# Kernel tuning notes

Hardware: AMD Instinct MI355X
Metric: run time of the kernel (lower is better)

## Reference

```python
import jax, jax.numpy as jnp
import numpy as np

DIM = 512
HEADS = 8
DH = 64
LANDMARKS = 256
PINV_ITERS = 6
K = 4
BUF = 256


def _ln(x, g, b, eps=1e-5):
    mu = x.mean(-1, keepdims=True)
    var = ((x - mu) ** 2).mean(-1, keepdims=True)
    return (x - mu) / jnp.sqrt(var + eps) * g + b


def _pinv(a):
    # Moore-Penrose iterative pseudo-inverse (lucidrains nystrom_attention)
    aa = jnp.abs(a)
    z = jnp.swapaxes(a, -1, -2) / (aa.sum(-1).max() * aa.sum(-2).max())
    I = jnp.eye(a.shape[-1], dtype=a.dtype)
    for _ in range(PINV_ITERS):
        az = a @ z
        z = 0.25 * z @ (13.0 * I - az @ (15.0 * I - az @ (7.0 * I - az)))
    return z


def _nystrom(x, qkv_w, out_w, out_b, res_k):
    b, n, _ = x.shape
    rem = n % LANDMARKS
    if rem > 0:
        x = jnp.pad(x, ((0, 0), (LANDMARKS - rem, 0), (0, 0)))  # left-pad seq
    npad = x.shape[1]
    qkv = x @ qkv_w.T
    q, k, v = jnp.split(qkv, 3, axis=-1)
    split_heads = lambda t: t.reshape(b, npad, HEADS, DH).transpose(0, 2, 1, 3)
    q = split_heads(q) * (DH ** -0.5)
    k = split_heads(k)
    v = split_heads(v)
    l = npad // LANDMARKS
    q_l = q.reshape(b, HEADS, LANDMARKS, l, DH).mean(3)
    k_l = k.reshape(b, HEADS, LANDMARKS, l, DH).mean(3)
    a1 = jax.nn.softmax(jnp.einsum('bhnd,bhmd->bhnm', q, k_l), axis=-1)
    a2 = jax.nn.softmax(jnp.einsum('bhmd,bhkd->bhmk', q_l, k_l), axis=-1)
    a3 = jax.nn.softmax(jnp.einsum('bhmd,bhnd->bhmn', q_l, k), axis=-1)
    out = (a1 @ _pinv(a2)) @ (a3 @ v)  # (b,h,npad,dh)
    # depthwise residual conv over seq dim, one channel per head
    out = out + jax.lax.conv_general_dilated(
        v, res_k, (1, 1), ((16, 16), (0, 0)),
        dimension_numbers=('NCHW', 'OIHW', 'NCHW'), feature_group_count=HEADS)
    out = out.transpose(0, 2, 1, 3).reshape(b, npad, DIM) @ out_w.T + out_b
    return out[:, -n:]


def _dwconv(x, w, b, pad):
    y = jax.lax.conv_general_dilated(
        x, w, (1, 1), ((pad, pad), (pad, pad)),
        dimension_numbers=('NCHW', 'OIHW', 'NCHW'), feature_group_count=DIM)
    return y + b[None, :, None, None]


def _leaky(t):
    return jnp.where(t >= 0, t, 0.01 * t)


def reference(x, fc1_w, fc1_b, cls_token, ln1_g, ln1_b, qkv1_w, out1_w, out1_b, res1_k,
              ppeg_w7, ppeg_b7, ppeg_w5, ppeg_b5, ppeg_w3, ppeg_b3,
              ln2_g, ln2_b, qkv2_w, out2_w, out2_b, res2_k, norm_g, norm_b, fc2_w, fc2_b,
              dsl_w1, dsl_b1, dsl_w2, dsl_b2,
              gcn_w1, gcn_we, gcn_b1, gcn_w2, gcn_b2,
              gcn_head_w, gcn_head_b, gcn_dist_w, gcn_dist_b, rehearsal):
    B, N, _ = x.shape
    h = jax.nn.relu(x @ fc1_w.T + fc1_b)                 # (B,N,512)
    Hs = int(np.ceil(np.sqrt(N)))                        # square-grid side
    add = Hs * Hs - N
    h = jnp.concatenate([h, h[:, :add]], axis=1)         # wrap-pad to Hs*Hs
    h = jnp.concatenate([jnp.broadcast_to(cls_token, (B, 1, DIM)), h], axis=1)
    h = h + _nystrom(_ln(h, ln1_g, ln1_b), qkv1_w, out1_w, out1_b, res1_k)
    cls, feat = h[:, :1], h[:, 1:]
    cnn = feat.transpose(0, 2, 1).reshape(B, DIM, Hs, Hs)
    cnn = cnn + _dwconv(cnn, ppeg_w7, ppeg_b7, 3) + _dwconv(cnn, ppeg_w5, ppeg_b5, 2) + _dwconv(cnn, ppeg_w3, ppeg_b3, 1)
    h = jnp.concatenate([cls, cnn.reshape(B, DIM, -1).transpose(0, 2, 1)], axis=1)
    h = h + _nystrom(_ln(h, ln2_g, ln2_b), qkv2_w, out2_w, out2_b, res2_k)
    h = _ln(h, norm_g, norm_b)[:, 0]                     # (B,512) cls embedding
    logits_mlp = h @ fc2_w.T + fc2_b
    # rehearsal concat -> buffer of BUF nodes
    x_concat = jnp.concatenate([h, rehearsal], axis=0)[:BUF]
    # DSL: MLP + cosine KNN graph + scatter_mean edge_attr
    xg = _leaky(_leaky(x_concat @ dsl_w1.T + dsl_b1) @ dsl_w2.T + dsl_b2)
    xn = xg / jnp.linalg.norm(xg, axis=-1, keepdims=True)
    _, idx = jax.lax.top_k(xn @ xn.T, K)                 # (BUF,K) cosine KNN incl self
    edge_attr = xg[idx].mean(1)                          # scatter_mean over incoming edges
    # 2-layer GCN over the KNN graph (mean aggregation + edge_attr injection)
    h1 = jax.nn.relu((xg + edge_attr) @ gcn_w1.T + edge_attr @ gcn_we.T + gcn_b1)
    h2 = (h1 + h1[idx].mean(1)) @ gcn_w2.T + gcn_b2
    logits_graph = h2[:B] @ gcn_head_w.T + gcn_head_b
    logits_distill = h1[:B] @ gcn_dist_w.T + gcn_dist_b
    return logits_mlp, logits_graph, logits_distill


def setup_inputs() -> dict:
    key = jax.random.key(0)
    ks = jax.random.split(key, 24)
    r = lambda i, shp, s=0.02: jax.random.normal(ks[i], shp, dtype=jnp.float32) * s
    z = lambda shp: jnp.zeros(shp, dtype=jnp.float32)
    o = lambda shp: jnp.ones(shp, dtype=jnp.float32)
    return {
        'x': jax.random.normal(ks[0], (2, 4096, 512), dtype=jnp.float32),
        'fc1_w': r(1, (512, 512)), 'fc1_b': z((512,)),
        'cls_token': r(2, (1, 1, 512), 1.0),
        'ln1_g': o((512,)), 'ln1_b': z((512,)),
        'qkv1_w': r(3, (1536, 512)), 'out1_w': r(4, (512, 512)), 'out1_b': z((512,)),
        'res1_k': r(5, (8, 1, 33, 1)),
        'ppeg_w7': r(6, (512, 1, 7, 7)), 'ppeg_b7': z((512,)),
        'ppeg_w5': r(7, (512, 1, 5, 5)), 'ppeg_b5': z((512,)),
        'ppeg_w3': r(8, (512, 1, 3, 3)), 'ppeg_b3': z((512,)),
        'ln2_g': o((512,)), 'ln2_b': z((512,)),
        'qkv2_w': r(9, (1536, 512)), 'out2_w': r(10, (512, 512)), 'out2_b': z((512,)),
        'res2_k': r(11, (8, 1, 33, 1)),
        'norm_g': o((512,)), 'norm_b': z((512,)),
        'fc2_w': r(12, (2, 512)), 'fc2_b': z((2,)),
        'dsl_w1': r(13, (256, 512)), 'dsl_b1': z((256,)),
        'dsl_w2': r(14, (512, 256)), 'dsl_b2': z((512,)),
        'gcn_w1': r(15, (512, 512)), 'gcn_we': r(16, (512, 512)), 'gcn_b1': z((512,)),
        'gcn_w2': r(17, (512, 512)), 'gcn_b2': z((512,)),
        'gcn_head_w': r(18, (2, 512)), 'gcn_head_b': z((2,)),
        'gcn_dist_w': r(19, (2, 512)), 'gcn_dist_b': z((2,)),
        'rehearsal': jax.random.uniform(ks[20], (256, 512), dtype=jnp.float32),
    }
```

## Files before the change

kernel.cpp:

```cpp
#include <hip/hip_runtime.h>
#include <math.h>

#define BB 2
#define NSEQ 4096
#define N1 4097
#define NPAD 4352
#define PADR 255
#define DIM 512
#define NH 8
#define DH 64
#define LM 256
#define NT 1536

typedef short bf16x8 __attribute__((ext_vector_type(8)));
typedef float f32x4 __attribute__((ext_vector_type(4)));

__device__ __forceinline__ unsigned short f2bf(float x){
  unsigned int u = __float_as_uint(x);
  unsigned int r = (u + 0x7FFFu + ((u >> 16) & 1u)) >> 16;
  return (unsigned short)r;
}
__device__ __forceinline__ float bf2f(unsigned short h){
  return __uint_as_float(((unsigned int)h) << 16);
}
// ... 138 lines not shown

#define DOMFMA2(AH_, AL_, BH_, BL_) do {                               \
    _Pragma("unroll")                                                  \
    for (int i = 0; i < 2; ++i)                                        \
      _Pragma("unroll")                                                \
      for (int j = 0; j < 2; ++j) {                                    \
        acc[i][j] = __builtin_amdgcn_mfma_f32_16x16x32_bf16(AH_[i], BH_[j], acc[i][j], 0,0,0); \
        acc[i][j] = __builtin_amdgcn_mfma_f32_16x16x32_bf16(AH_[i], BL_[j], acc[i][j], 0,0,0); \
        acc[i][j] = __builtin_amdgcn_mfma_f32_16x16x32_bf16(AL_[i], BH_[j], acc[i][j], 0,0,0); \
      } } while (0)

  LDF2(A0h, A0l, B0h, B0l, 0);
  for (int ks = 0; ks < 256; ks += 64) {
    LDF2(A1h, A1l, B1h, B1l, ks + 32);
    DOMFMA2(A0h, A0l, B0h, B0l);
    if (ks + 64 < 256) LDF2(A0h, A0l, B0h, B0l, ks + 64);
    DOMFMA2(A1h, A1l, B1h, B1l);
  }
#undef LDF2
#undef DOMFMA2

  int crb = (l >> 4) << 2;
  #pragma unroll
  for (int i = 0; i < 2; ++i) {
    int rbase = row0 + i*16 + crb;
    #pragma unroll
    for (int j = 0; j < 2; ++j) {
      int colg = col0 + j*16 + lr;
      float v[4];
      #pragma unroll
      for (int r = 0; r < 4; ++r)
        v[r] = alpha * acc[i][j][r] + (((rbase + r) == colg) ? diag : 0.f);
      if (C32) {
        #pragma unroll
        for (int r = 0; r < 4; ++r) C32[offC + (size_t)(rbase + r) * N + colg] = v[r];
      }
      if (CH) {
        #pragma unroll
        for (int r = 0; r < 4; ++r) {
          unsigned short hh = f2bf(v[r]);
          CH[offC + (size_t)(rbase + r) * N + colg] = hh;
          CL[offC + (size_t)(rbase + r) * N + colg] = f2bf(v[r] - bf2f(hh));
        }
      }
      if (CTH) {
        ushort4 th, tl;
        unsigned short* ph = (unsigned short*)&th;
        unsigned short* pl = (unsigned short*)&tl;
        #pragma unroll
        for (int r = 0; r < 4; ++r) { ph[r] = f2bf(v[r]); pl[r] = f2bf(v[r] - bf2f(ph[r])); }
        *(ushort4*)&CTH[offT + (size_t)colg * 256 + rbase] = th;
        *(ushort4*)&CTL[offT + (size_t)colg * 256 + rbase] = tl;
      }
      if (DTH) {
        ushort4 th, tl;
        unsigned short* ph = (unsigned short*)&th;
        unsigned short* pl = (unsigned short*)&tl;
        #pragma unroll
        for (int r = 0; r < 4; ++r) {
          float dv = (((rbase + r) == colg) ? diag2 : 0.f) - v[r];
          ph[r] = f2bf(dv); pl[r] = f2bf(dv - bf2f(ph[r]));
        }
        *(ushort4*)&DTH[offT + (size_t)colg * 256 + rbase] = th;
        *(ushort4*)&DTL[offT + (size_t)colg * 256 + rbase] = tl;
      }
    }
  }
}

__global__ void split_k(const float* __restrict__ src, unsigned short* __restrict__ dh,
                        unsigned short* __restrict__ dl, int n4){
  int i = blockIdx.x * 256 + threadIdx.x;
  if (i >= n4) return;
  float4 v = ((const float4*)src)[i];
  ushort4 H, L;
  H.x = f2bf(v.x); L.x = f2bf(v.x - bf2f(H.x));
  H.y = f2bf(v.y); L.y = f2bf(v.y - bf2f(H.y));
  H.z = f2bf(v.z); L.z = f2bf(v.z - bf2f(H.z));
  H.w = f2bf(v.w); L.w = f2bf(v.w - bf2f(H.w));
  ((ushort4*)dh)[i] = H;
  ((ushort4*)dl)[i] = L;
}

__global__ void z0_split(const float* __restrict__ a2, const float* __restrict__ scal,
                         unsigned short* __restrict__ zH, unsigned short* __restrict__ zL,
                         unsigned short* __restrict__ zTH, unsigned short* __restrict__ zTL){
  size_t idx = (size_t)blockIdx.x * 256 + threadIdx.x;
  size_t bh = idx >> 16;
  int rc = (int)(idx & 65535);
  int r = rc >> 8, c = rc & 255;
  float v = a2[idx] * scal[32];
  unsigned short hh = f2bf(v), ll = f2bf(v - bf2f(hh));
  zTH[idx] = hh; zTL[idx] = ll;
  size_t tidx = (bh << 16) + (size_t)c * 256 + r;
  zH[tidx] = hh; zL[tidx] = ll;
}

__global__ void split_T_av(const float* __restrict__ av,
                           unsigned short* __restrict__ TH, unsigned short* __restrict__ TL){
  size_t idx = (size_t)blockIdx.x * 256 + threadIdx.x;
  size_t bh = idx >> 14;
  int md = (int)(idx & 16383);
  int m = md >> 6, d = md & 63;
  float v = av[idx];
  unsigned short hh = f2bf(v);
  size_t tix = (bh << 14) + (size_t)d * 256 + m;
  TH[tix] = hh; TL[tix] = f2bf(v - bf2f(hh));
}

__global__ __launch_bounds__(256) void ln_pad_split(const float* __restrict__ hsrc,
    unsigned short* __restrict__ dH, unsigned short* __restrict__ dL,
    const float* __restrict__ g, const float* __restrict__ bt){
  __shared__ double red[256];
  int row = blockIdx.x;
  int b = row / NPAD, r = row % NPAD;
  unsigned short* rh = dH + (size_t)row * DIM;
  unsigned short* rl = dL + (size_t)row * DIM;
  int t = threadIdx.x;
  if (r < PADR) { rh[t] = 0; rh[t+256] = 0; rl[t] = 0; rl[t+256] = 0; return; }
  const float* x = hsrc + ((size_t)b * N1 + (r - PADR)) * DIM;
  double x0 = (double)x[t], x1 = (double)x[t + 256];
  double mu = blk_sumd(x0 + x1, red) * (1.0/512.0);
  double d0 = x0 - mu, d1 = x1 - mu;
  double var = blk_sumd(d0*d0 + d1*d1, red) * (1.0/512.0);
  double inv = 1.0 / sqrt(var + 1e-5);
  float y0 = (float)(d0 * inv * (double)g[t]       + (double)bt[t]);
  float y1 = (float)(d1 * inv * (double)g[t + 256] + (double)bt[t + 256]);
  unsigned short h0 = f2bf(y0), h1 = f2bf(y1);
  rh[t] = h0;       rl[t] = f2bf(y0 - bf2f(h0));
  rh[t + 256] = h1; rl[t + 256] = f2bf(y1 - bf2f(h1));
}

__global__ void landmark(const float* __restrict__ qkv, float* __restrict__ ql, float* __restrict__ kl){
  int blk = blockIdx.x;
  int bh = blk >> 8, m = blk & 255;
  int b = bh >> 3, hh = bh & 7;
  int d = threadIdx.x;
  float sq = 0.f, sk = 0.f;
  for (int l = 0; l < 17; ++l) {
    size_t o = ((size_t)b * NPAD + m * 17 + l) * NT + hh * 64 + d;
    sq += qkv[o];
    sk += qkv[o + 512];
  }
  ql[((size_t)bh * 256 + m) * 64 + d] = 0.125f * sq / 17.f;
  kl[((size_t)bh * 256 + m) * 64 + d] = sk / 17.f;
}

__global__ __launch_bounds__(256) void transpose_kl(const float* __restrict__ kl, float* __restrict__ klT){
  __shared__ float tile[64][65];
  int bh = blockIdx.y;
  int m0 = blockIdx.x * 64;
  int t = threadIdx.x;
  for (int i = t; i < 4096; i += 256) {
    int r = i >> 6, c = i & 63;
    tile[r][c] = kl[((size_t)bh * 256 + m0 + r) * 64 + c];
  }
  __syncthreads();
  float* kb = klT + (size_t)bh * 64 * 256;
  for (int i = t; i < 4096; i += 256) {
    int d = i >> 6, mm = i & 63;
    kb[(size_t)d * 256 + m0 + mm] = tile[mm][d];
  }
}

__global__ __launch_bounds__(256) void a2_kernel(const float* __restrict__ ql, const float* __restrict__ klT,
                                                 float* __restrict__ a2){
  __shared__ float qs[64]; __shared__ float red[256];
  int blk = blockIdx.x;
  int bh = blk >> 8, i = blk & 255;
  int t = threadIdx.x;
  if (t < 64) qs[t] = ql[((size_t)bh * 256 + i) * 64 + t];
  __syncthreads();
  const float* kb = klT + (size_t)bh * 16384;
  float s = 0.f;
  #pragma unroll
  for (int d = 0; d < 64; ++d) s += qs[d] * kb[d * 256 + t];
  float mx = blk_max(s, red);
  float e = expf(s - mx);
  float sum = blk_sum(e, red);
  a2[((size_t)bh * 256 + i) * 256 + t] = e / sum;
}

__global__ __launch_bounds__(256) void colrow_max(const float* __restrict__ a2, float* __restrict__ scal){
  __shared__ float red[256];
  int bh = blockIdx.x, t = threadIdx.x;
  const float* A = a2 + (size_t)bh * 65536;
  float cs = 0.f, rs = 0.f;
  for (int i = 0; i < 256; ++i) cs += A[(size_t)i * 256 + t];
  for (int j = 0; j < 256; ++j) rs += A[(size_t)t * 256 + j];
  float cmax = blk_max(cs, red);
  float rmax = blk_max(rs, red);
  if (t == 0) { scal[bh] = cmax; scal[16 + bh] = rmax; }
}
__global__ void scal_red(float* scal){
  if (threadIdx.x == 0) {
    float cm = scal[0], rm = scal[16];
    for (int i = 1; i < 16; ++i) { cm = fmaxf(cm, scal[i]); rm = fmaxf(rm, scal[16 + i]); }
    scal[32] = 1.f / (rm * cm);
  }
}

__global__ __launch_bounds__(256) void fa3v_kernel(const float* __restrict__ qkv, const float* __restrict__ ql,
                                                   float* __restrict__ accp, float* __restrict__ mlp){
  int part = blockIdx.x, qt = blockIdx.y, bh = blockIdx.z;
  int b = bh >> 3, hh = bh & 7;
  int t = threadIdx.x;
  int w = t >> 6, l = t & 63;
  int lr = l & 15, lk = (l >> 4) << 3;
  int w16 = w * 16;
  int crb = (l >> 4) << 2;
  __shared__ unsigned short KH[64][72], KL[64][72];
  __shared__ unsigned short PH[64][72], PL[64][72];
  __shared__ float Ss[64][68];
  __shared__ float redm[64][4];
  __shared__ float mrow[64], lrow[64], scales[64];
  bf16x8 qh[2], qlo[2];
  {
    const float* qrow = ql + ((size_t)bh * 256 + qt * 64 + w16 + lr) * 64;
    #pragma unroll
    for (int s = 0; s < 2; ++s) {
      #pragma unroll
      for (int e = 0; e < 8; ++e) {
        float v = qrow[s * 32 + lk + e];
        unsigned short hv = f2bf(v);
        qh[s][e]  = (short)hv;
        qlo[s][e] = (short)f2bf(v - bf2f(hv));
      }
    }
  }
  if (t < 64) { mrow[t] = -3.4e38f; lrow[t] = 0.f; }
  f32x4 acc[4];
  #pragma unroll
  for (int j = 0; j < 4; ++j) acc[j] = (f32x4){0.f,0.f,0.f,0.f};
  __syncthreads();
  int rr = t >> 2, sg = (t & 3) << 4;
  for (int tile = 0; tile < 4; ++tile) {
    int nbase = part * 256 + tile * 64;
    for (int i = t; i < 4096; i += 256) {
      int r = i >> 6, c = i & 63;
      float v = qkv[((size_t)b * NPAD + nbase + r) * NT + 512 + hh * 64 + c];
      unsigned short hv = f2bf(v);
      KH[r][c] = hv; KL[r][c] = f2bf(v - bf2f(hv));
    }
    __syncthreads();
    #pragma unroll
    for (int j = 0; j < 4; ++j) {
      f32x4 sf = (f32x4){0.f,0.f,0.f,0.f};
      #pragma unroll
      for (int s = 0; s < 2; ++s) {
        bf16x8 kh8 = *(const bf16x8*)&KH[j*16 + lr][s*32 + lk];
        bf16x8 kl8 = *(const bf16x8*)&KL[j*16 + lr][s*32 + lk];
        sf = __builtin_amdgcn_mfma_f32_16x16x32_bf16(qh[s],  kh8, sf, 0,0,0);
        sf = __builtin_amdgcn_mfma_f32_16x16x32_bf16(qh[s],  kl8, sf, 0,0,0);
        sf = __builtin_amdgcn_mfma_f32_16x16x32_bf16(qlo[s], kh8, sf, 0,0,0);
      }
      #pragma unroll
      for (int r = 0; r < 4; ++r) Ss[w16 + crb + r][j*16 + lr] = sf[r];
    }
    __syncthreads();
    for (int i = t; i < 4096; i += 256) {
      int r = i >> 6, c = i & 63;
      float v = qkv[((size_t)b * NPAD + nbase + r) * NT + 1024 + hh * 64 + c];
      unsigned short hv = f2bf(v);
      KH[c][r] = hv; KL[c][r] = f2bf(v - bf2f(hv));
    }
    float lm = -3.4e38f;
    #pragma unroll
    for (int c = 0; c < 16; ++c) lm = fmaxf(lm, Ss[rr][sg + c]);
    redm[rr][t & 3] = lm;
    float mold = mrow[rr];
    float rm = fmaxf(fmaxf(redm[rr][0], redm[rr][1]), fmaxf(redm[rr][2], redm[rr][3]));
    float mnew = fmaxf(mold, rm);
    float sc_r = expf(mold - mnew);
    if ((t & 3) == 0) { scales[rr] = sc_r; mrow[rr] = mnew; }
    float ls = 0.f;
    #pragma unroll
    for (int c = 0; c < 16; ++c) {
      float p = expf(Ss[rr][sg + c] - mnew);
      unsigned short hv = f2bf(p);
      PH[rr][sg + c] = hv; PL[rr][sg + c] = f2bf(p - bf2f(hv));
      ls += p;
    }
    redm[rr][t & 3] = ls;
    __syncthreads();
    if ((t & 3) == 0) lrow[rr] = lrow[rr] * sc_r + redm[rr][0]+redm[rr][1]+redm[rr][2]+redm[rr][3];
    {
      float s0 = scales[w16 + crb], s1 = scales[w16 + crb + 1],
            s2 = scales[w16 + crb + 2], s3 = scales[w16 + crb + 3];
      #pragma unroll
      for (int j = 0; j < 4; ++j) { acc[j][0]*=s0; acc[j][1]*=s1; acc[j][2]*=s2; acc[j][3]*=s3; }
    }
    bf16x8 pah[2], pal[2];
    #pragma unroll
    for (int s = 0; s < 2; ++s) {
      pah[s] = *(const bf16x8*)&PH[w16 + lr][s*32 + lk];
      pal[s] = *(const bf16x8*)&PL[w16 + lr][s*32 + lk];
    }
    #pragma unroll
    for (int j = 0; j < 4; ++j) {
      #pragma unroll
      for (int s = 0; s < 2; ++s) {
        bf16x8 vh = *(const bf16x8*)&KH[j*16 + lr][s*32 + lk];
        bf16x8 vl = *(const bf16x8*)&KL[j*16 + lr][s*32 + lk];
        acc[j] = __builtin_amdgcn_mfma_f32_16x16x32_bf16(pah[s], vh, acc[j], 0,0,0);
        acc[j] = __builtin_amdgcn_mfma_f32_16x16x32_bf16(pah[s], vl, acc[j], 0,0,0);
        acc[j] = __builtin_amdgcn_mfma_f32_16x16x32_bf16(pal[s], vh, acc[j], 0,0,0);
      }
    }
    __syncthreads();
  }
  int blk = (bh * 4 + qt) * 17 + part;
  float* ap = accp + (size_t)blk * 4096;
  #pragma unroll
  for (int j = 0; j < 4; ++j)
    #pragma unroll
    for (int r = 0; r < 4; ++r)
      ap[(w16 + crb + r) * 64 + j*16 + lr] = acc[j][r];
  if (t < 64) { mlp[(size_t)blk*128 + t] = mrow[t]; mlp[(size_t)blk*128 + 64 + t] = lrow[t]; }
}

__global__ __launch_bounds__(256) void fa3v_combine(const float* __restrict__ accp, const float* __restrict__ mlp,
                                                    float* __restrict__ av){
  int g = blockIdx.x;
  int t = threadIdx.x;
  int r = t >> 2, sg = (t & 3) << 4;
  int bh = g >> 2, qt = g & 3;
  float mp[17], lp[17];
  #pragma unroll
  for (int p = 0; p < 17; ++p) {
    mp[p] = mlp[(size_t)(g*17+p)*128 + r];
    lp[p] = mlp[(size_t)(g*17+p)*128 + 64 + r];
  }
  float M = mp[0];
  #pragma unroll
  for (int p = 1; p < 17; ++p) M = fmaxf(M, mp[p]);
  float w[17]; float L = 0.f;
  #pragma unroll
  for (int p = 0; p < 17; ++p) { w[p] = expf(mp[p] - M); L += w[p] * lp[p]; }
  float invL = 1.f / L;
  #pragma unroll
  for (int c = 0; c < 16; ++c) {
    float s = 0.f;
    #pragma unroll
    for (int p = 0; p < 17; ++p) s += w[p] * accp[(size_t)(g*17+p)*4096 + r*64 + sg + c];
    av[((size_t)(bh*256 + qt*64 + r))*64 + sg + c] = s * invL;
  }
}

__global__ __launch_bounds__(256) void fa1_kernel(const float* __restrict__ qkv, const float* __restrict__ kl,
                                                  const float* __restrict__ zav, float* __restrict__ merged,
                                                  unsigned short* __restrict__ merH,
                                                  unsigned short* __restrict__ merL){
  int nt = blockIdx.x, bh = blockIdx.y;
  int b = bh >> 3, hh = bh & 7;
  int t = threadIdx.x;
  int w = t >> 6, l = t & 63;
  int lr = l & 15, lk = (l >> 4) << 3;
  int w16 = w * 16;
  int crb = (l >> 4) << 2;
  int n0 = nt * 64;
  __shared__ unsigned short KH[64][72], KL[64][72];
  __shared__ unsigned short PH[64][72], PL[64][72];
  __shared__ float Ss[64][68];
  __shared__ float redm[64][4];
  __shared__ float mrow[64], lrow[64], scales[64];
  bf16x8 qh[2], qlo[2];
  {
    const float* qrow = qkv + ((size_t)b * NPAD + n0 + w16 + lr) * NT + hh * 64;
    #pragma unroll
    for (int s = 0; s < 2; ++s) {
      #pragma unroll
      for (int e = 0; e < 8; ++e) {
        float v = 0.125f * qrow[s * 32 + lk + e];
        unsigned short hv = f2bf(v);
        qh[s][e]  = (short)hv;
        qlo[s][e] = (short)f2bf(v - bf2f(hv));
      }
    }
  }
  if (t < 64) { mrow[t] = -3.4e38f; lrow[t] = 0.f; }
  f32x4 acc[4];
  #pragma unroll
  for (int j = 0; j < 4; ++j) acc[j] = (f32x4){0.f,0.f,0.f,0.f};
  __syncthreads();
  int rr = t >> 2, sg = (t & 3) << 4;
  for (int tile = 0; tile < 4; ++tile) {
    int mbase = tile * 64;
    for (int i = t; i < 4096; i += 256) {
      int r = i >> 6, c = i & 63;
      float v = kl[((size_t)bh * 256 + mbase + r) * 64 + c];
      unsigned short hv = f2bf(v);
      KH[r][c] = hv; KL[r][c] = f2bf(v - bf2f(hv));
    }
    __syncthreads();
    #pragma unroll
    for (int j = 0; j < 4; ++j) {
      f32x4 sf = (f32x4){0.f,0.f,0.f,0.f};
      #pragma unroll
      for (int s = 0; s < 2; ++s) {
        bf16x8 kh8 = *(const bf16x8*)&KH[j*16 + lr][s*32 + lk];
        bf16x8 kl8 = *(const bf16x8*)&KL[j*16 + lr][s*32 + lk];
        sf = __builtin_amdgcn_mfma_f32_16x16x32_bf16(qh[s],  kh8, sf, 0,0,0);
        sf = __builtin_amdgcn_mfma_f32_16x16x32_bf16(qh[s],  kl8, sf, 0,0,0);
        sf = __builtin_amdgcn_mfma_f32_16x16x32_bf16(qlo[s], kh8, sf, 0,0,0);
      }
      #pragma unroll
      for (int r = 0; r < 4; ++r) Ss[w16 + crb + r][j*16 + lr] = sf[r];
    }
    __syncthreads();
    for (int i = t; i < 4096; i += 256) {
      int r = i >> 6, c = i & 63;
      float v = zav[((size_t)bh * 256 + mbase + r) * 64 + c];
      unsigned short hv = f2bf(v);
      KH[c][r] = hv; KL[c][r] = f2bf(v - bf2f(hv));
    }
    float lm = -3.4e38f;
    #pragma unroll
    for (int c = 0; c < 16; ++c) lm = fmaxf(lm, Ss[rr][sg + c]);
    redm[rr][t & 3] = lm;
    float mold = mrow[rr];
    float rm = fmaxf(fmaxf(redm[rr][0], redm[rr][1]), fmaxf(redm[rr][2], redm[rr][3]));
    float mnew = fmaxf(mold, rm);
    float sc_r = expf(mold - mnew);
    if ((t & 3) == 0) { scales[rr] = sc_r; mrow[rr] = mnew; }
    float ls = 0.f;
    #pragma unroll
    for (int c = 0; c < 16; ++c) {
      float p = expf(Ss[rr][sg + c] - mnew);
      unsigned short hv = f2bf(p);
      PH[rr][sg + c] = hv; PL[rr][sg + c] = f2bf(p - bf2f(hv));
      ls += p;
    }
    redm[rr][t & 3] = ls;
    __syncthreads();
    if ((t & 3) == 0) lrow[rr] = lrow[rr] * sc_r + redm[rr][0]+redm[rr][1]+redm[rr][2]+redm[rr][3];
    {
      float s0 = scales[w16 + crb], s1 = scales[w16 + crb + 1],
            s2 = scales[w16 + crb + 2], s3 = scales[w16 + crb + 3];
      #pragma unroll
      for (int j = 0; j < 4; ++j) { acc[j][0]*=s0; acc[j][1]*=s1; acc[j][2]*=s2; acc[j][3]*=s3; }
    }
    bf16x8 pah[2], pal[2];
    #pragma unroll
    for (int s = 0; s < 2; ++s) {
      pah[s] = *(const bf16x8*)&PH[w16 + lr][s*32 + lk];
      pal[s] = *(const bf16x8*)&PL[w16 + lr][s*32 + lk];
    }
    #pragma unroll
    for (int j = 0; j < 4; ++j) {
      #pragma unroll
      for (int s = 0; s < 2; ++s) {
        bf16x8 vh = *(const bf16x8*)&KH[j*16 + lr][s*32 + lk];
        bf16x8 vl = *(const bf16x8*)&KL[j*16 + lr][s*32 + lk];
        acc[j] = __builtin_amdgcn_mfma_f32_16x16x32_bf16(pah[s], vh, acc[j], 0,0,0);
        acc[j] = __builtin_amdgcn_mfma_f32_16x16x32_bf16(pah[s], vl, acc[j], 0,0,0);
        acc[j] = __builtin_amdgcn_mfma_f32_16x16x32_bf16(pal[s], vh, acc[j], 0,0,0);
      }
    }
    __syncthreads();
  }
  #pragma unroll
  for (int r = 0; r < 4; ++r) {
    float invl = 1.f / lrow[w16 + crb + r];
    size_t rowoff = ((size_t)b * NPAD + n0 + w16 + crb + r) * DIM + hh * 64;
    float* mp = &merged[rowoff];
    #pragma unroll
    for (int j = 0; j < 4; ++j) {
      float v = mp[j*16 + lr] + acc[j][r] * invl;
      mp[j*16 + lr] = v;
      unsigned short hv = f2bf(v);
      merH[rowoff + j*16 + lr] = hv;
      merL[rowoff + j*16 + lr] = f2bf(v - bf2f(hv));
    }
  }
}

__global__ __launch_bounds__(256) void conv_res(const float* __restrict__ qkv, const float* __restrict__ rk,
                                                float* __restrict__ merged){
  __shared__ float vt[288][16];
  __shared__ float rks[33];
  int n0 = blockIdx.x * 256;
  int c0 = blockIdx.y * 16;
  int b  = blockIdx.z;
  int t = threadIdx.x;
  int hh = c0 >> 6;
  if (t < 33) rks[t] = rk[hh * 33 + t];
  for (int i = t; i < 288 * 4; i += 256) {
    int sp = i >> 2, q = (i & 3) << 2;
    int n = n0 - 16 + sp;
    float4 v = make_float4(0.f,0.f,0.f,0.f);
    if (n >= 0 && n < NPAD)
      v = *(const float4*)&qkv[((size_t)b * NPAD + n) * NT + 1024 + c0 + q];
    vt[sp][q] = v.x; vt[sp][q+1] = v.y; vt[sp][q+2] = v.z; vt[sp][q+3] = v.w;
  }
  __syncthreads();
  int c = t & 15, g = t >> 4;
  for (int m = 0; m < 16; ++m) {
// ... 92 lines not shown
  __shared__ double red[256];
  int i = blockIdx.x, t = threadIdx.x;
  double a = (double)xg[(size_t)i * 512 + t], b = (double)xg[(size_t)i * 512 + t + 256];
  double s = blk_sumd(a*a + b*b, red);
  if (t == 0) rn[i] = sqrt(s);
}

__global__ __launch_bounds__(256) void topk_k(const float* __restrict__ xg, const double* __restrict__ rn,
                                              int* __restrict__ idxb){
  __shared__ double sc[256]; __shared__ double redv[256]; __shared__ int redi[256];
  int i = blockIdx.x, j = threadIdx.x;
  const float* xi = xg + (size_t)i * 512;
  const float* xj = xg + (size_t)j * 512;
  double s = 0.;
  for (int c = 0; c < 512; ++c) s += (double)xi[c] * (double)xj[c];
  s /= (rn[i] * rn[j]);
  sc[j] = s; __syncthreads();
  for (int r = 0; r < 4; ++r) {
    redv[j] = sc[j]; redi[j] = j; __syncthreads();
    for (int st = 128; st > 0; st >>= 1) {
      if (j < st) {
        if (redv[j + st] > redv[j] || (redv[j + st] == redv[j] && redi[j + st] < redi[j])) {
          redv[j] = redv[j + st]; redi[j] = redi[j + st];
        }
      }
      __syncthreads();
    }
    if (j == 0) { idxb[i * 4 + r] = redi[0]; sc[redi[0]] = -1e300; }
    __syncthreads();
  }
}

__global__ void edge_k_split(const float* __restrict__ xg, const int* __restrict__ idxb,
                             float* __restrict__ edge,
                             unsigned short* __restrict__ eH, unsigned short* __restrict__ eL){
  size_t idx = (size_t)blockIdx.x * 256 + threadIdx.x;
  int i = (int)(idx >> 9), c = (int)(idx & 511);
  const int* id = idxb + i * 4;
  float v = 0.25f * (xg[(size_t)id[0]*512 + c] + xg[(size_t)id[1]*512 + c] +
                     xg[(size_t)id[2]*512 + c] + xg[(size_t)id[3]*512 + c]);
  edge[idx] = v;
  unsigned short hh = f2bf(v);
  eH[idx] = hh; eL[idx] = f2bf(v - bf2f(hh));
}
__global__ void vadd_split(const float* __restrict__ a, const float* __restrict__ b,
                           unsigned short* __restrict__ oH, unsigned short* __restrict__ oL){
  size_t idx = (size_t)blockIdx.x * 256 + threadIdx.x;
  float v = a[idx] + b[idx];
  unsigned short hh = f2bf(v);
  oH[idx] = hh; oL[idx] = f2bf(v - bf2f(hh));
}
__global__ void h1gather_split(const float* __restrict__ h1, const int* __restrict__ idxb,
                               unsigned short* __restrict__ oH, unsigned short* __restrict__ oL){
  size_t idx = (size_t)blockIdx.x * 256 + threadIdx.x;
  int i = (int)(idx >> 9), c = (int)(idx & 511);
  const int* id = idxb + i * 4;
  float v = h1[idx] + 0.25f * (h1[(size_t)id[0]*512 + c] + h1[(size_t)id[1]*512 + c] +
                               h1[(size_t)id[2]*512 + c] + h1[(size_t)id[3]*512 + c]);
  unsigned short hh = f2bf(v);
  oH[idx] = hh; oL[idx] = f2bf(v - bf2f(hh));
}

__global__ void logits2(const float* __restrict__ src, const float* __restrict__ w,
                        const float* __restrict__ bias, float* __restrict__ out){
  int rc = blockIdx.x; int r = rc >> 1, c = rc & 1;
  int t = threadIdx.x;
  double s = 0.;
  for (int k = t; k < 512; k += 64) s += (double)src[(size_t)r * 512 + k] * (double)w[(size_t)c * 512 + k];
  for (int off = 32; off > 0; off >>= 1) s += __shfl_down(s, off);
  if (t == 0) out[rc] = (float)(s + (double)bias[c]);
}

__global__ void sentinel_k(float* out){ if (threadIdx.x < 12) out[threadIdx.x] = 1e30f; }

struct NysBufs {
  float *qkv, *ql, *kl, *klT, *av, *zav, *merged;
  float *a2f32, *scal, *accp, *mlp;
  unsigned short *padH, *padL, *merH, *merL, *wqH, *wqL, *owH, *owL;
  unsigned short *a2H, *a2L;
  unsigned short *zAH, *zAL, *zATH, *zATL;
  unsigned short *zBH, *zBL, *zBTH, *zBTL;
  unsigned short *azH, *azL, *t1TH, *t1TL, *t2TH, *t2TL;
  unsigned short *avTH, *avTL;
};

static void run_nystrom(hipStream_t stream, float* hbuf,
                        const float* lng, const float* lnb, const float* qkvw,
                        const float* outw, const float* outb, const float* rk,
                        const NysBufs& w)
{
  ln_pad_split<<<BB * NPAD, 256, 0, stream>>>(hbuf, w.padH, w.padL, lng, lnb);
  split_k<<<(NT * DIM / 4 + 255) / 256, 256, 0, stream>>>(qkvw, w.wqH, w.wqL, NT * DIM / 4);
  gemm_mfma<<<dim3(NT/128, (BB*NPAD)/128), 256, 0, stream>>>(w.padH, w.padL, w.wqH, w.wqL,
                                                             nullptr, nullptr, w.qkv,
                                                             BB*NPAD, NT, DIM, 0, nullptr, nullptr);
  landmark<<<BB * NH * LM, 64, 0, stream>>>(w.qkv, w.ql, w.kl);
  transpose_kl<<<dim3(LM/64, 16), 256, 0, stream>>>(w.kl, w.klT);
  fa3v_kernel<<<dim3(17, 4, 16), 256, 0, stream>>>(w.qkv, w.ql, w.accp, w.mlp);
  fa3v_combine<<<64, 256, 0, stream>>>(w.accp, w.mlp, w.av);
  split_T_av<<<1024, 256, 0, stream>>>(w.av, w.avTH, w.avTL);
  a2_kernel<<<BB * NH * LM, 256, 0, stream>>>(w.ql, w.klT, w.a2f32);
  colrow_max<<<16, 256, 0, stream>>>(w.a2f32, w.scal);
  scal_red<<<1, 64, 0, stream>>>(w.scal);
  split_k<<<(16 * 65536 / 4 + 255) / 256, 256, 0, stream>>>(w.a2f32, w.a2H, w.a2L, 16 * 65536 / 4);
  z0_split<<<4096, 256, 0, stream>>>(w.a2f32, w.scal, w.zAH, w.zAL, w.zATH, w.zATL);
  const unsigned short *zcH = w.zAH, *zcL = w.zAL, *zcTH = w.zATH, *zcTL = w.zATL;
  unsigned short *znH = w.zBH, *znL = w.zBL, *znTH = w.zBTH, *znTL = w.zBTL;
  for (int it = 0; it < 6; ++it) {
    mm_mfma<<<dim3(8,8,16), 64, 0, stream>>>(w.a2H, w.a2L, zcTH, zcTL,
        w.azH, w.azL, nullptr, nullptr, w.t1TH, w.t1TL, nullptr, 256, 1.f, 0.f, 7.f);
    mm_mfma<<<dim3(8,8,16), 64, 0, stream>>>(w.azH, w.azL, w.t1TH, w.t1TL,
        nullptr, nullptr, w.t2TH, w.t2TL, nullptr, nullptr, nullptr, 256, -1.f, 15.f, 0.f);
    mm_mfma<<<dim3(8,8,16), 64, 0, stream>>>(w.azH, w.azL, w.t2TH, w.t2TL,
        nullptr, nullptr, w.t1TH, w.t1TL, nullptr, nullptr, nullptr, 256, -1.f, 13.f, 0.f);
    mm_mfma<<<dim3(8,8,16), 64, 0, stream>>>(zcH, zcL, w.t1TH, w.t1TL,
        znH, znL, znTH, znTL, nullptr, nullptr, nullptr, 256, 0.25f, 0.f, 0.f);
    const unsigned short* t;
    t = zcH; zcH = znH; znH = (unsigned short*)t;
    t = zcL; zcL = znL; znL = (unsigned short*)t;
    t = zcTH; zcTH = znTH; znTH = (unsigned short*)t;
    t = zcTL; zcTL = znTL; znTL = (unsigned short*)t;
  }
  mm_mfma<<<dim3(2,8,16), 64, 0, stream>>>(zcH, zcL, w.avTH, w.avTL,
      nullptr, nullptr, nullptr, nullptr, nullptr, nullptr, w.zav, 64, 1.f, 0.f, 0.f);
  conv_res<<<dim3(17, 32, 2), 256, 0, stream>>>(w.qkv, rk, w.merged);
  fa1_kernel<<<dim3(NPAD/64, 16), 256, 0, stream>>>(w.qkv, w.kl, w.zav, w.merged, w.merH, w.merL);
  split_k<<<(DIM*DIM/4 + 255) / 256, 256, 0, stream>>>(outw, w.owH, w.owL, DIM*DIM/4);
  for (int b = 0; b < BB; ++b)
    gemm_mfma<<<dim3(DIM/128, (N1+127)/128), 256, 0, stream>>>(
        w.merH + ((size_t)b*NPAD + PADR)*DIM, w.merL + ((size_t)b*NPAD + PADR)*DIM,
        w.owH, w.owL, outb,
        hbuf + (size_t)b*N1*DIM, hbuf + (size_t)b*N1*DIM,
        N1, DIM, DIM, 0, nullptr, nullptr);
}

extern "C" void kernel_launch(void* const* d_in, const int* in_sizes, int n_in,
                              void* d_out, int out_size, void* d_ws, size_t ws_size,
                              hipStream_t stream) {
  (void)in_sizes; (void)n_in; (void)out_size;
  const float* x        = (const float*)d_in[0];
  const float* fc1_w    = (const float*)d_in[1];
  const float* fc1_b    = (const float*)d_in[2];
  const float* cls_tok  = (const float*)d_in[3];
  const float* ln1_g    = (const float*)d_in[4];
  const float* ln1_b    = (const float*)d_in[5];
  const float* qkv1_w   = (const float*)d_in[6];
  const float* out1_w   = (const float*)d_in[7];
  const float* out1_b   = (const float*)d_in[8];
  const float* res1_k   = (const float*)d_in[9];
  const float* ppeg_w7  = (const float*)d_in[10];
  const float* ppeg_b7  = (const float*)d_in[11];
  const float* ppeg_w5  = (const float*)d_in[12];
  const float* ppeg_b5  = (const float*)d_in[13];
  const float* ppeg_w3  = (const float*)d_in[14];
  const float* ppeg_b3  = (const float*)d_in[15];
  const float* ln2_g    = (const float*)d_in[16];
  const float* ln2_b    = (const float*)d_in[17];
  const float* qkv2_w   = (const float*)d_in[18];
  const float* out2_w   = (const float*)d_in[19];
  const float* out2_b   = (const float*)d_in[20];
  const float* res2_k   = (const float*)d_in[21];
  const float* norm_g   = (const float*)d_in[22];
  const float* norm_b   = (const float*)d_in[23];
  const float* fc2_w    = (const float*)d_in[24];
  const float* fc2_b    = (const float*)d_in[25];
  const float* dsl_w1   = (const float*)d_in[26];
  const float* dsl_b1   = (const float*)d_in[27];
  const float* dsl_w2   = (const float*)d_in[28];
  const float* dsl_b2   = (const float*)d_in[29];
  const float* gcn_w1   = (const float*)d_in[30];
  const float* gcn_we   = (const float*)d_in[31];
  const float* gcn_b1   = (const float*)d_in[32];
  const float* gcn_w2   = (const float*)d_in[33];
  const float* gcn_b2   = (const float*)d_in[34];
  const float* gcn_hw   = (const float*)d_in[35];
  const float* gcn_hb   = (const float*)d_in[36];
  const float* gcn_dw   = (const float*)d_in[37];
  const float* gcn_db   = (const float*)d_in[38];
  const float* rehearsal= (const float*)d_in[39];
  float* out = (float*)d_out;

  char* base = (char*)d_ws;
  size_t off = 0;
  auto takeb = [&](size_t bytes) { void* p = base + off; off += (bytes + 255) & ~(size_t)255; return p; };

  float* h    = (float*)takeb((size_t)BB * N1 * DIM * 4);
  float* h2   = (float*)takeb((size_t)BB * N1 * DIM * 4);
  NysBufs nb;
  nb.padH   = (unsigned short*)takeb((size_t)BB * NPAD * DIM * 2);
  nb.padL   = (unsigned short*)takeb((size_t)BB * NPAD * DIM * 2);
  nb.qkv    = (float*)takeb((size_t)BB * NPAD * NT * 4);
  nb.ql     = (float*)takeb((size_t)BB * NH * LM * DH * 4);
  nb.kl     = (float*)takeb((size_t)BB * NH * LM * DH * 4);
  nb.klT    = (float*)takeb((size_t)BB * NH * LM * DH * 4);
  nb.av     = (float*)takeb((size_t)BB * NH * LM * DH * 4);
  nb.zav    = (float*)takeb((size_t)BB * NH * LM * DH * 4);
  nb.merged = (float*)takeb((size_t)BB * NPAD * DIM * 4);
  nb.merH   = (unsigned short*)takeb((size_t)BB * NPAD * DIM * 2);
  nb.merL   = (unsigned short*)takeb((size_t)BB * NPAD * DIM * 2);
  nb.wqH    = (unsigned short*)takeb((size_t)NT * DIM * 2);
  nb.wqL    = (unsigned short*)takeb((size_t)NT * DIM * 2);
  nb.owH    = (unsigned short*)takeb((size_t)DIM * DIM * 2);
  nb.owL    = (unsigned short*)takeb((size_t)DIM * DIM * 2);
  nb.avTH   = (unsigned short*)takeb((size_t)16 * 64 * 256 * 2);
  nb.avTL   = (unsigned short*)takeb((size_t)16 * 64 * 256 * 2);
  nb.scal   = (float*)takeb(64 * 4);
  nb.mlp    = (float*)takeb((size_t)1088 * 128 * 4);
  float* hcls = (float*)takeb((size_t)BB * DIM * 4);
  float* xg1  = (float*)takeb((size_t)256 * 256 * 4);
  float* xg   = (float*)takeb((size_t)256 * 512 * 4);
  double* rn  = (double*)takeb(256 * 8);
  int*   idxb = (int*)takeb(1024 * 4);
  float* edge = (float*)takeb((size_t)256 * 512 * 4);
  float* h1g  = (float*)takeb((size_t)256 * 512 * 4);
  float* h2g  = (float*)takeb((size_t)256 * 512 * 4);
  unsigned short* xcH   = (unsigned short*)takeb((size_t)256 * 512 * 2);
  unsigned short* xcL   = (unsigned short*)takeb((size_t)256 * 512 * 2);
  unsigned short* dw1H  = (unsigned short*)takeb((size_t)256 * 512 * 2);
  unsigned short* dw1L  = (unsigned short*)takeb((size_t)256 * 512 * 2);
  unsigned short* xg1H  = (unsigned short*)takeb((size_t)256 * 256 * 2);
  unsigned short* xg1L  = (unsigned short*)takeb((size_t)256 * 256 * 2);
  unsigned short* dw2H  = (unsigned short*)takeb((size_t)512 * 256 * 2);
  unsigned short* dw2L  = (unsigned short*)takeb((size_t)512 * 256 * 2);
  unsigned short* h1pH  = (unsigned short*)takeb((size_t)256 * 512 * 2);
  unsigned short* h1pL  = (unsigned short*)takeb((size_t)256 * 512 * 2);
  unsigned short* gw1H  = (unsigned short*)takeb((size_t)512 * 512 * 2);
  unsigned short* gw1L  = (unsigned short*)takeb((size_t)512 * 512 * 2);
  unsigned short* edgeH = (unsigned short*)takeb((size_t)256 * 512 * 2);
  unsigned short* edgeL = (unsigned short*)takeb((size_t)256 * 512 * 2);
  unsigned short* gweH  = (unsigned short*)takeb((size_t)512 * 512 * 2);
  unsigned short* gweL  = (unsigned short*)takeb((size_t)512 * 512 * 2);
  unsigned short* h1p2H = (unsigned short*)takeb((size_t)256 * 512 * 2);
  unsigned short* h1p2L = (unsigned short*)takeb((size_t)256 * 512 * 2);
  unsigned short* gw2H  = (unsigned short*)takeb((size_t)512 * 512 * 2);
  unsigned short* gw2L  = (unsigned short*)takeb((size_t)512 * 512 * 2);

  const size_t MB2 = (size_t)16 * 65536;
  unsigned short* pr = nb.padH;
  nb.a2H  = pr;            nb.a2L  = pr + MB2;
  nb.zAH  = pr + 2*MB2;    nb.zAL  = pr + 3*MB2;
  nb.zATH = pr + 4*MB2;    nb.zATL = pr + 5*MB2;
  nb.azH  = pr + 6*MB2;    nb.azL  = pr + 7*MB2;
  unsigned short* mr = (unsigned short*)nb.merged;
  nb.zBH  = mr;            nb.zBL  = mr + MB2;
  nb.zBTH = mr + 2*MB2;    nb.zBTL = mr + 3*MB2;
  nb.t1TH = mr + 4*MB2;    nb.t1TL = mr + 5*MB2;
  nb.t2TH = mr + 6*MB2;    nb.t2TL = mr + 7*MB2;
  nb.a2f32 = (float*)(mr + 4*MB2);
  nb.accp  = nb.merged;

  if (ws_size < off) { sentinel_k<<<1, 64, 0, stream>>>(out); return; }

  set_cls<<<1, 1024, 0, stream>>>(h, cls_tok);
  split_k<<<(BB*NSEQ*DIM/4 + 255) / 256, 256, 0, stream>>>(x, nb.merH, nb.merL, BB*NSEQ*DIM/4);
  split_k<<<(DIM*DIM/4 + 255) / 256, 256, 0, stream>>>(fc1_w, nb.owH, nb.owL, DIM*DIM/4);
  for (int b = 0; b < BB; ++b)
    gemm_mfma<<<dim3(DIM/128, NSEQ/128), 256, 0, stream>>>(
        nb.merH + (size_t)b*NSEQ*DIM, nb.merL + (size_t)b*NSEQ*DIM,
        nb.owH, nb.owL, fc1_b, nullptr,
        h + ((size_t)b*N1 + 1)*DIM, NSEQ, DIM, DIM, 1, nullptr, nullptr);
  run_nystrom(stream, h, ln1_g, ln1_b, qkv1_w, out1_w, out1_b, res1_k, nb);

  copy_cls<<<1, 1024, 0, stream>>>(h2, h);
  dwconv<<<dim3(16, 32, 2), 256, 0, stream>>>(h, ppeg_w7, ppeg_b7, ppeg_w5, ppeg_b5,
                                              ppeg_w3, ppeg_b3, h2);
  run_nystrom(stream, h2, ln2_g, ln2_b, qkv2_w, out2_w, out2_b, res2_k, nb);

  final_ln<<<BB, 256, 0, stream>>>(h2, norm_g, norm_b, hcls);
  logits2<<<4, 64, 0, stream>>>(hcls, fc2_w, fc2_b, out + 0);

  build_xc_split<<<512, 256, 0, stream>>>(hcls, rehearsal, xcH, xcL);
  split_k<<<(256*512/4 + 255) / 256, 256, 0, stream>>>(dsl_w1, dw1H, dw1L, 256*512/4);
  split_k<<<(512*256/4 + 255) / 256, 256, 0, stream>>>(dsl_w2, dw2H, dw2L, 512*256/4);
  split_k<<<(512*512/4 + 255) / 256, 256, 0, stream>>>(gcn_w1, gw1H, gw1L, 512*512/4);
  split_k<<<(512*512/4 + 255) / 256, 256, 0, stream>>>(gcn_we, gweH, gweL, 512*512/4);
  split_k<<<(512*512/4 + 255) / 256, 256, 0, stream>>>(gcn_w2, gw2H, gw2L, 512*512/4);
  gemm_mfma<<<dim3(2, 2), 256, 0, stream>>>(xcH, xcL, dw1H, dw1L, dsl_b1, nullptr,
                                            xg1, 256, 256, 512, 2, xg1H, xg1L);
  gemm_mfma<<<dim3(4, 2), 256, 0, stream>>>(xg1H, xg1L, dw2H, dw2L, dsl_b2, nullptr,
                                            xg, 256, 512, 256, 2, nullptr, nullptr);
  norms_k<<<256, 256, 0, stream>>>(xg, rn);
  topk_k<<<256, 256, 0, stream>>>(xg, rn, idxb);
  edge_k_split<<<512, 256, 0, stream>>>(xg, idxb, edge, edgeH, edgeL);
  vadd_split<<<512, 256, 0, stream>>>(xg, edge, h1pH, h1pL);
  gemm_mfma<<<dim3(4, 2), 256, 0, stream>>>(h1pH, h1pL, gw1H, gw1L, nullptr, nullptr,
                                            h1g, 256, 512, 512, 0, nullptr, nullptr);
  gemm_mfma<<<dim3(4, 2), 256, 0, stream>>>(edgeH, edgeL, gweH, gweL, gcn_b1, h1g,
                                            h1g, 256, 512, 512, 1, nullptr, nullptr);
  h1gather_split<<<512, 256, 0, stream>>>(h1g, idxb, h1p2H, h1p2L);
  gemm_mfma<<<dim3(4, 2), 256, 0, stream>>>(h1p2H, h1p2L, gw2H, gw2L, gcn_b2, nullptr,
                                            h2g, 256, 512, 512, 0, nullptr, nullptr);
  logits2<<<4, 64, 0, stream>>>(h2g, gcn_hw, gcn_hb, out + 4);
  logits2<<<4, 64, 0, stream>>>(h1g, gcn_dw, gcn_db, out + 8);
}
```

Before: 1.873 ms.

## Pre-split K/V into bf16 hi/lo layouts before attention kernels

Adds kernels that convert K and V from the fp32 qkv buffer into bf16 hi/lo pairs once, with V and zav stored transposed. fa3v and fa1 can then load tiles with 16-byte vector loads instead of per-element fp32 loads, conversions and strided transposed shared-memory stores. The conversion was previously repeated for every query tile. In exchange it adds extra passes over K and V and reuses the padH/merH workspace buffers, which relies on their lifetimes not overlapping.

New measurement: 1.752 ms. 1.07x faster.

```diff
diff --git a/kernel.cpp b/kernel.cpp
--- a/kernel.cpp
+++ b/kernel.cpp
@@ -244,6 +244,42 @@
   ((ushort4*)dl)[i] = L;
 }
 
+__global__ void split_kcols(const float* __restrict__ qkv,
+                            unsigned short* __restrict__ dh, unsigned short* __restrict__ dl){
+  size_t idx = (size_t)blockIdx.x * 256 + threadIdx.x;
+  size_t row = idx >> 7;
+  int c4 = (int)(idx & 127) << 2;
+  float4 v = *(const float4*)&qkv[row * NT + 512 + c4];
+  ushort4 H, L;
+  H.x = f2bf(v.x); L.x = f2bf(v.x - bf2f(H.x));
+  H.y = f2bf(v.y); L.y = f2bf(v.y - bf2f(H.y));
+  H.z = f2bf(v.z); L.z = f2bf(v.z - bf2f(H.z));
+  H.w = f2bf(v.w); L.w = f2bf(v.w - bf2f(H.w));
+  *(ushort4*)&dh[row * 512 + c4] = H;
+  *(ushort4*)&dl[row * 512 + c4] = L;
+}
+
+__global__ __launch_bounds__(256) void transpose_split_v(const float* __restrict__ qkv,
+    unsigned short* __restrict__ VTH, unsigned short* __restrict__ VTL){
+  __shared__ float tile[64][65];
+  int bh = blockIdx.y;
+  int n0 = blockIdx.x * 64;
+  int b = bh >> 3, hh = bh & 7;
+  int t = threadIdx.x;
+  for (int i = t; i < 4096; i += 256) {
+    int r = i >> 6, c = i & 63;
+    tile[r][c] = qkv[((size_t)b * NPAD + n0 + r) * NT + 1024 + hh * 64 + c];
+  }
+  __syncthreads();
+  for (int i = t; i < 4096; i += 256) {
+    int d = i >> 6, n = i & 63;
+    float v = tile[n][d];
+    unsigned short hv = f2bf(v);
+    size_t o = ((size_t)bh * 64 + d) * NPAD + n0 + n;
+    VTH[o] = hv; VTL[o] = f2bf(v - bf2f(hv));
+  }
+}
+
 __global__ void z0_split(const float* __restrict__ a2, const float* __restrict__ scal,
                          unsigned short* __restrict__ zH, unsigned short* __restrict__ zL,
                          unsigned short* __restrict__ zTH, unsigned short* __restrict__ zTL){
@@ -362,7 +398,11 @@
   }
 }
 
-__global__ __launch_bounds__(256) void fa3v_kernel(const float* __restrict__ qkv, const float* __restrict__ ql,
+__global__ __launch_bounds__(256) void fa3v_kernel(const unsigned short* __restrict__ KsH,
+                                                   const unsigned short* __restrict__ KsL,
+                                                   const unsigned short* __restrict__ VTH,
+                                                   const unsigned short* __restrict__ VTL,
+                                                   const float* __restrict__ ql,
                                                    float* __restrict__ accp, float* __restrict__ mlp){
   int part = blockIdx.x, qt = blockIdx.y, bh = blockIdx.z;
   int b = bh >> 3, hh = bh & 7;
@@ -398,11 +438,16 @@
   int rr = t >> 2, sg = (t & 3) << 4;
   for (int tile = 0; tile < 4; ++tile) {
     int nbase = part * 256 + tile * 64;
-    for (int i = t; i < 4096; i += 256) {
-      int r = i >> 6, c = i & 63;
-      float v = qkv[((size_t)b * NPAD + nbase + r) * NT + 512 + hh * 64 + c];
-      unsigned short hv = f2bf(v);
-      KH[r][c] = hv; KL[r][c] = f2bf(v - bf2f(hv));
+    {
+      const unsigned short* kbH = KsH + ((size_t)b * NPAD + nbase) * 512 + hh * 64;
+      const unsigned short* kbL = KsL + ((size_t)b * NPAD + nbase) * 512 + hh * 64;
+      #pragma unroll
+      for (int u = 0; u < 2; ++u) {
+        int i = t + u * 256;
+        int r = i >> 3, c8 = (i & 7) << 3;
+        *(bf16x8*)&KH[r][c8] = *(const bf16x8*)(kbH + (size_t)r * 512 + c8);
+        *(bf16x8*)&KL[r][c8] = *(const bf16x8*)(kbL + (size_t)r * 512 + c8);
+      }
     }
     __syncthreads();
     #pragma unroll
@@ -420,11 +465,16 @@
       for (int r = 0; r < 4; ++r) Ss[w16 + crb + r][j*16 + lr] = sf[r];
     }
     __syncthreads();
-    for (int i = t; i < 4096; i += 256) {
-      int r = i >> 6, c = i & 63;
-      float v = qkv[((size_t)b * NPAD + nbase + r) * NT + 1024 + hh * 64 + c];
-      unsigned short hv = f2bf(v);
-      KH[c][r] = hv; KL[c][r] = f2bf(v - bf2f(hv));
+    {
+      const unsigned short* vbH = VTH + (size_t)bh * 64 * NPAD + nbase;
+      const unsigned short* vbL = VTL + (size_t)bh * 64 * NPAD + nbase;
+      #pragma unroll
+      for (int u = 0; u < 2; ++u) {
+        int i = t + u * 256;
+        int d = i >> 3, c8 = (i & 7) << 3;
+        *(bf16x8*)&KH[d][c8] = *(const bf16x8*)(vbH + (size_t)d * NPAD + c8);
+        *(bf16x8*)&KL[d][c8] = *(const bf16x8*)(vbL + (size_t)d * NPAD + c8);
+      }
     }
     float lm = -3.4e38f;
     #pragma unroll
@@ -509,8 +559,12 @@
   }
 }
 
-__global__ __launch_bounds__(256) void fa1_kernel(const float* __restrict__ qkv, const float* __restrict__ kl,
-                                                  const float* __restrict__ zav, float* __restrict__ merged,
+__global__ __launch_bounds__(256) void fa1_kernel(const float* __restrict__ qkv,
+                                                  const unsigned short* __restrict__ klsH,
+                                                  const unsigned short* __restrict__ klsL,
+                                                  const unsigned short* __restrict__ zavTH,
+                                                  const unsigned short* __restrict__ zavTL,
+                                                  float* __restrict__ merged,
                                                   unsigned short* __restrict__ merH,
                                                   unsigned short* __restrict__ merL){
   int nt = blockIdx.x, bh = blockIdx.y;
@@ -548,11 +602,16 @@
   int rr = t >> 2, sg = (t & 3) << 4;
   for (int tile = 0; tile < 4; ++tile) {
     int mbase = tile * 64;
-    for (int i = t; i < 4096; i += 256) {
-      int r = i >> 6, c = i & 63;
-      float v = kl[((size_t)bh * 256 + mbase + r) * 64 + c];
-      unsigned short hv = f2bf(v);
-      KH[r][c] = hv; KL[r][c] = f2bf(v - bf2f(hv));
+    {
+      const unsigned short* kbH = klsH + ((size_t)bh * 256 + mbase) * 64;
+      const unsigned short* kbL = klsL + ((size_t)bh * 256 + mbase) * 64;
+      #pragma unroll
+      for (int u = 0; u < 2; ++u) {
+        int i = t + u * 256;
+        int r = i >> 3, c8 = (i & 7) << 3;
+        *(bf16x8*)&KH[r][c8] = *(const bf16x8*)(kbH + (size_t)r * 64 + c8);
+        *(bf16x8*)&KL[r][c8] = *(const bf16x8*)(kbL + (size_t)r * 64 + c8);
+      }
     }
     __syncthreads();
     #pragma unroll
@@ -570,11 +629,16 @@
       for (int r = 0; r < 4; ++r) Ss[w16 + crb + r][j*16 + lr] = sf[r];
     }
     __syncthreads();
-    for (int i = t; i < 4096; i += 256) {
-      int r = i >> 6, c = i & 63;
-      float v = zav[((size_t)bh * 256 + mbase + r) * 64 + c];
-      unsigned short hv = f2bf(v);
-      KH[c][r] = hv; KL[c][r] = f2bf(v - bf2f(hv));
+    {
+      const unsigned short* vbH = zavTH + (size_t)bh * 64 * 256 + mbase;
+      const unsigned short* vbL = zavTL + (size_t)bh * 64 * 256 + mbase;
+      #pragma unroll
+      for (int u = 0; u < 2; ++u) {
+        int i = t + u * 256;
+        int d = i >> 3, c8 = (i & 7) << 3;
+        *(bf16x8*)&KH[d][c8] = *(const bf16x8*)(vbH + (size_t)d * 256 + c8);
+        *(bf16x8*)&KL[d][c8] = *(const bf16x8*)(vbL + (size_t)d * 256 + c8);
+      }
     }
     float lm = -3.4e38f;
     #pragma unroll
@@ -833,6 +897,8 @@
   unsigned short *zBH, *zBL, *zBTH, *zBTL;
   unsigned short *azH, *azL, *t1TH, *t1TL, *t2TH, *t2TL;
   unsigned short *avTH, *avTL;
+  unsigned short *KsH, *KsL, *VTH, *VTL;
+  unsigned short *klsH, *klsL, *zavTH, *zavTL;
 };
 
 static void run_nystrom(hipStream_t stream, float* hbuf,
@@ -845,9 +911,12 @@
   gemm_mfma<<<dim3(NT/128, (BB*NPAD)/128), 256, 0, stream>>>(w.padH, w.padL, w.wqH, w.wqL,
                                                              nullptr, nullptr, w.qkv,
                                                              BB*NPAD, NT, DIM, 0, nullptr, nullptr);
+  split_kcols<<<BB * NPAD * 128 / 256, 256, 0, stream>>>(w.qkv, w.KsH, w.KsL);
+  transpose_split_v<<<dim3(NPAD/64, 16), 256, 0, stream>>>(w.qkv, w.VTH, w.VTL);
   landmark<<<BB * NH * LM, 64, 0, stream>>>(w.qkv, w.ql, w.kl);
   transpose_kl<<<dim3(LM/64, 16), 256, 0, stream>>>(w.kl, w.klT);
-  fa3v_kernel<<<dim3(17, 4, 16), 256, 0, stream>>>(w.qkv, w.ql, w.accp, w.mlp);
+  split_k<<<(16 * LM * DH / 4 + 255) / 256, 256, 0, stream>>>(w.kl, w.klsH, w.klsL, 16 * LM * DH / 4);
+  fa3v_kernel<<<dim3(17, 4, 16), 256, 0, stream>>>(w.KsH, w.KsL, w.VTH, w.VTL, w.ql, w.accp, w.mlp);
   fa3v_combine<<<64, 256, 0, stream>>>(w.accp, w.mlp, w.av);
   split_T_av<<<1024, 256, 0, stream>>>(w.av, w.avTH, w.avTL);
   a2_kernel<<<BB * NH * LM, 256, 0, stream>>>(w.ql, w.klT, w.a2f32);
@@ -874,8 +943,10 @@
   }
   mm_mfma<<<dim3(2,8,16), 64, 0, stream>>>(zcH, zcL, w.avTH, w.avTL,
       nullptr, nullptr, nullptr, nullptr, nullptr, nullptr, w.zav, 64, 1.f, 0.f, 0.f);
+  split_T_av<<<1024, 256, 0, stream>>>(w.zav, w.zavTH, w.zavTL);
   conv_res<<<dim3(17, 32, 2), 256, 0, stream>>>(w.qkv, rk, w.merged);
-  fa1_kernel<<<dim3(NPAD/64, 16), 256, 0, stream>>>(w.qkv, w.kl, w.zav, w.merged, w.merH, w.merL);
+  fa1_kernel<<<dim3(NPAD/64, 16), 256, 0, stream>>>(w.qkv, w.klsH, w.klsL, w.zavTH, w.zavTL,
+                                                    w.merged, w.merH, w.merL);
   split_k<<<(DIM*DIM/4 + 255) / 256, 256, 0, stream>>>(outw, w.owH, w.owL, DIM*DIM/4);
   for (int b = 0; b < BB; ++b)
     gemm_mfma<<<dim3(DIM/128, (N1+127)/128), 256, 0, stream>>>(
@@ -955,6 +1026,10 @@
   nb.owL    = (unsigned short*)takeb((size_t)DIM * DIM * 2);
   nb.avTH   = (unsigned short*)takeb((size_t)16 * 64 * 256 * 2);
   nb.avTL   = (unsigned short*)takeb((size_t)16 * 64 * 256 * 2);
+  nb.klsH   = (unsigned short*)takeb((size_t)16 * LM * DH * 2);
+  nb.klsL   = (unsigned short*)takeb((size_t)16 * LM * DH * 2);
+  nb.zavTH  = (unsigned short*)takeb((size_t)16 * 64 * 256 * 2);
+  nb.zavTL  = (unsigned short*)takeb((size_t)16 * 64 * 256 * 2);
   nb.scal   = (float*)takeb(64 * 4);
   nb.mlp    = (float*)takeb((size_t)1088 * 128 * 4);
   float* hcls = (float*)takeb((size_t)BB * DIM * 4);
@@ -999,6 +1074,10 @@
   nb.t2TH = mr + 6*MB2;    nb.t2TL = mr + 7*MB2;
   nb.a2f32 = (float*)(mr + 4*MB2);
   nb.accp  = nb.merged;
+  nb.KsH = nb.padH;
+  nb.KsL = nb.padL;
+  nb.VTH = nb.merH;
+  nb.VTL = nb.merL;
 
   if (ws_size < off) { sentinel_k<<<1, 64, 0, stream>>>(out); return; }
 
```
